# Kernel optimization log

Measured on AMD Instinct MI355X. Metric: run time of the kernel, lower is better.

## Reference

```python
import jax, jax.numpy as jnp
import numpy as np

HEAD_DIM = 64
MASK_PENALTY = 1000000.0


def setup_inputs() -> dict:
    key = jax.random.key(0)
    kq, kk, kv, ki = jax.random.split(key, 4)
    B, H, S, D = 32, 16, 512, HEAD_DIM
    E, CAP = 8, 4  # n_experts = hidden(1024)//128, capacity per expert
    Q = jax.random.normal(kq, (B, H, S, D), dtype=jnp.float32)
    K = jax.random.normal(kk, (B, H, S, D), dtype=jnp.float32)
    V = jax.random.normal(kv, (B, H, S, D), dtype=jnp.float32)
    idx_list = jax.random.randint(ki, (E, CAP), 0, B)  # per-expert routed batch indices
    mask = jnp.ones((B, S), dtype=jnp.float32)
    return {"Q": Q, "K": K, "V": V, "idx_list": idx_list, "mask": mask}


def reference(Q, K, V, idx_list, mask):
    # Per-expert grouped attention: gather routed batch rows, QK^T, masked
    # softmax, AV. Dropout is identity in eval mode.
    scale = 1.0 / jnp.sqrt(jnp.asarray(HEAD_DIM, dtype=Q.dtype))

    def expert_attn(idx_e):
        q = Q[idx_e]            # [cap, H, S, D]
        k = K[idx_e]
        v = V[idx_e]
        m = mask[idx_e]         # [cap, S]
        dot = jnp.einsum('bhsd,bhtd->bhst', q, k) * scale
        dot = dot - MASK_PENALTY * (1.0 - m[:, None, None, :])
        p = jax.nn.softmax(dot, axis=-1)
        return jnp.einsum('bhst,bhtd->bhsd', p, v)  # [cap, H, S, D]

    X = jax.vmap(expert_attn)(idx_list)  # [E, cap, H, S, D]
    return X
```

## Files before the change

kernel.cpp:

```cpp
#include <hip/hip_runtime.h>
#include <math.h>


typedef _Float16 f16x8 __attribute__((ext_vector_type(8)));
typedef _Float16 f16x4 __attribute__((ext_vector_type(4)));
typedef _Float16 f16x2 __attribute__((ext_vector_type(2)));
typedef float    f32x4 __attribute__((ext_vector_type(4)));

#define MFMA16(a, b, c) __builtin_amdgcn_mfma_f32_16x16x32_f16((a), (b), (c), 0, 0, 0)

constexpr int Hh = 16;
constexpr int Ss = 512;
constexpr int Dd = 64;
constexpr int QB = 256;
constexpr int KVB = 64;
constexpr int NT = Ss / KVB;
constexpr float QS = 0.125f * 1.44269504088896f;
constexpr float BM = 1000000.0f * 1.44269504088896f;

union U8 { f16x8 v; f16x2 h[4]; };

__device__ __forceinline__ int SW(int row, int col) {
  return row * 64 + (col ^ ((row & 7) << 3));
}

__device__ __forceinline__ f16x2 pkrtz(float a, float b) {
  auto t = __builtin_amdgcn_cvt_pkrtz(a, b);
  return *(f16x2*)&t;
}

__global__ __launch_bounds__(512) void sparse_attn_kernel(
    const float* __restrict__ Q, const float* __restrict__ K,
    const float* __restrict__ V, const int* __restrict__ idx,
    const float* __restrict__ mask, float* __restrict__ out) {
  const int tid  = threadIdx.x;
  const int lane = tid & 63;
  const int wv   = tid >> 6;
  const int r    = lane & 15;
  const int g    = lane >> 4;

  const int phys = blockIdx.x;
  const int G    = (phys & 7) | ((phys >> 4) << 3);
  const int qb   = (phys >> 3) & 1;
  const int h    = G & 15;
  const int ec   = G >> 4;
  const int b    = idx[ec];

  __shared__ _Float16 Ks[64 * 64];
  __shared__ _Float16 VTs[64 * 64];
  __shared__ float    biasS[Ss];

  const size_t bh = ((size_t)b * Hh + h) * (size_t)Ss * Dd;
  const float* Qb = Q + bh;
  const float* Kb = K + bh;
  const float* Vb = V + bh;
  const float* mrow = mask + (size_t)b * Ss;

  biasS[tid] = mrow[tid] * BM - BM;

  const int q0 = qb * QB + wv * 32;

  f16x8 qf[2][2];
#pragma unroll
  for (int mi = 0; mi < 2; ++mi)
#pragma unroll
    for (int kk = 0; kk < 2; ++kk) {
      const float* qp = Qb + (size_t)(q0 + mi * 16 + r) * Dd + kk * 32 + g * 8;
      float4 x0 = *(const float4*)qp;
      float4 x1 = *(const float4*)(qp + 4);
      U8 u;
      u.h[0] = pkrtz(x0.x * QS, x0.y * QS);
      u.h[1] = pkrtz(x0.z * QS, x0.w * QS);
      u.h[2] = pkrtz(x1.x * QS, x1.y * QS);
      u.h[3] = pkrtz(x1.z * QS, x1.w * QS);
      qf[mi][kk] = u.v;
    }

  f16x8 ones;
#pragma unroll
  for (int e = 0; e < 8; ++e) ones[e] = (_Float16)1.0f;

  f32x4 oacc[2][4];
#pragma unroll
  for (int mi = 0; mi < 2; ++mi)
#pragma unroll
    for (int nj = 0; nj < 4; ++nj) oacc[mi][nj] = (f32x4){0.f, 0.f, 0.f, 0.f};
  f32x4 lacc[2] = {(f32x4){0.f, 0.f, 0.f, 0.f}, (f32x4){0.f, 0.f, 0.f, 0.f}};

  float4 kx0, kx1;
  float  vv[8];

#define KV_ISSUE(KV0)                                                        \
  {                                                                          \
    const float* kp_ = Kb + (size_t)((KV0) + (tid >> 3)) * Dd + (tid & 7) * 8;\
    kx0 = *(const float4*)kp_;                                               \
    kx1 = *(const float4*)(kp_ + 4);                                         \
    int oct = tid >> 6;                                                      \
    int kb1 = (oct >> 2) * 16 + (oct & 3) * 4;                               \
    const float* vp = Vb + (size_t)((KV0) + kb1) * Dd + (tid & 63);          \
    _Pragma("unroll")                                                        \
    for (int jj = 0; jj < 4; ++jj) {                                         \
      vv[jj]     = vp[(size_t)jj * Dd];                                      \
      vv[jj + 4] = vp[(size_t)(jj + 32) * Dd];                               \
    }                                                                        \
  }

#define STAGE_WRITE()                                                        \
  {                                                                          \
    U8 u;                                                                    \
    u.h[0] = pkrtz(kx0.x, kx0.y);                                            \
    u.h[1] = pkrtz(kx0.z, kx0.w);                                            \
    u.h[2] = pkrtz(kx1.x, kx1.y);                                            \
    u.h[3] = pkrtz(kx1.z, kx1.w);                                            \
    *(f16x8*)&Ks[SW(tid >> 3, (tid & 7) * 8)] = u.v;                         \
    U8 u2;                                                                   \
    u2.h[0] = pkrtz(vv[0], vv[1]);                                           \
    u2.h[1] = pkrtz(vv[2], vv[3]);                                           \
    u2.h[2] = pkrtz(vv[4], vv[5]);                                           \
    u2.h[3] = pkrtz(vv[6], vv[7]);                                           \
    *(f16x8*)&VTs[SW(tid & 63, (tid >> 6) * 8)] = u2.v;                      \
  }

  KV_ISSUE(0)

  for (int t = 0; t < NT; ++t) {
    const int kv0 = t * KVB;
    if (t) __syncthreads();

    STAGE_WRITE()
    if (t < NT - 1) KV_ISSUE(kv0 + KVB)
    __syncthreads();

    f32x4 bv[4];
#pragma unroll
    for (int nj = 0; nj < 4; ++nj)
      bv[nj] = *(const f32x4*)&biasS[kv0 + nj * 16 + g * 4];

    f32x4 sf[2][4];
#pragma unroll
    for (int nj = 0; nj < 4; ++nj) { sf[0][nj] = bv[nj]; sf[1][nj] = bv[nj]; }
    __builtin_amdgcn_s_setprio(1);
#pragma unroll
    for (int nj = 0; nj < 4; ++nj)
#pragma unroll
      for (int kk = 0; kk < 2; ++kk) {
        f16x8 kf = *(const f16x8*)&Ks[SW(nj * 16 + r, kk * 32 + g * 8)];
        sf[0][nj] = MFMA16(kf, qf[0][kk], sf[0][nj]);
        sf[1][nj] = MFMA16(kf, qf[1][kk], sf[1][nj]);
      }
    __builtin_amdgcn_s_setprio(0);

    f16x8 pf[2][2];
#pragma unroll
    for (int mi = 0; mi < 2; ++mi) {
      float p[4][4];
#pragma unroll
      for (int nj = 0; nj < 4; ++nj)
#pragma unroll
        for (int rg = 0; rg < 4; ++rg)
          p[nj][rg] = __builtin_amdgcn_exp2f(sf[mi][nj][rg]);
#pragma unroll
      for (int kk = 0; kk < 2; ++kk) {
        U8 u;
        u.h[0] = pkrtz(p[kk][0], p[kk][1]);
        u.h[1] = pkrtz(p[kk][2], p[kk][3]);
        u.h[2] = pkrtz(p[kk + 2][0], p[kk + 2][1]);
        u.h[3] = pkrtz(p[kk + 2][2], p[kk + 2][3]);
        pf[mi][kk] = u.v;
      }
    }

    __builtin_amdgcn_s_setprio(1);
#pragma unroll
    for (int kk = 0; kk < 2; ++kk) {
      lacc[0] = MFMA16(pf[0][kk], ones, lacc[0]);
      lacc[1] = MFMA16(pf[1][kk], ones, lacc[1]);
#pragma unroll
      for (int nj = 0; nj < 4; ++nj) {
        f16x8 vf = *(const f16x8*)&VTs[SW(nj * 16 + r, kk * 32 + g * 8)];
        oacc[0][nj] = MFMA16(pf[0][kk], vf, oacc[0][nj]);
        oacc[1][nj] = MFMA16(pf[1][kk], vf, oacc[1][nj]);
      }
    }
    __builtin_amdgcn_s_setprio(0);
  }

  float* ob = out + ((size_t)ec * Hh + h) * (size_t)Ss * Dd;
#pragma unroll
  for (int mi = 0; mi < 2; ++mi) {
    float i4[4];
#pragma unroll
    for (int rg = 0; rg < 4; ++rg) i4[rg] = 1.0f / lacc[mi][rg];
#pragma unroll
    for (int nj = 0; nj < 4; ++nj)
#pragma unroll
      for (int rg = 0; rg < 4; ++rg) {
        int row = q0 + mi * 16 + g * 4 + rg;
        int dim = nj * 16 + r;
        ob[(size_t)row * Dd + dim] = oacc[mi][nj][rg] * i4[rg];
      }
  }
}

extern "C" void kernel_launch(void* const* d_in, const int* in_sizes, int n_in,
                              void* d_out, int out_size, void* d_ws, size_t ws_size,
                              hipStream_t stream) {
  const float* Q    = (const float*)d_in[0];
  const float* K    = (const float*)d_in[1];
  const float* V    = (const float*)d_in[2];
  const int*   idx  = (const int*)d_in[3];
  const float* mask = (const float*)d_in[4];
  float* out = (float*)d_out;
  dim3 grid(1024), block(512);
  hipLaunchKernelGGL(sparse_attn_kernel, grid, block, 0, stream,
                     Q, K, V, idx, mask, out);
}
```

Measured before the change: 65.11 us.

## Split K and V staging into separate phases to overlap with compute

Separates the K and V global-load/LDS-stage steps so V for the current tile is staged while QK^T and softmax run, and K for the next tile is staged after the PV MFMAs. K is prefetched two tiles ahead, while V gets a one-tile prefetch. The barriers are moved so each shared buffer is written only after its readers finish. This aims to hide global-load latency and barrier stalls behind MFMA work, at the cost of a more delicate sync ordering.

```diff
diff --git a/kernel.cpp b/kernel.cpp
--- a/kernel.cpp
+++ b/kernel.cpp
@@ -3,7 +3,6 @@
 
 
 typedef _Float16 f16x8 __attribute__((ext_vector_type(8)));
-typedef _Float16 f16x4 __attribute__((ext_vector_type(4)));
 typedef _Float16 f16x2 __attribute__((ext_vector_type(2)));
 typedef float    f32x4 __attribute__((ext_vector_type(4)));
 
@@ -90,11 +89,15 @@
   float4 kx0, kx1;
   float  vv[8];
 
-#define KV_ISSUE(KV0)                                                        \
+#define K_ISSUE(KV0)                                                         \
   {                                                                          \
     const float* kp_ = Kb + (size_t)((KV0) + (tid >> 3)) * Dd + (tid & 7) * 8;\
     kx0 = *(const float4*)kp_;                                               \
     kx1 = *(const float4*)(kp_ + 4);                                         \
+  }
+
+#define V_ISSUE(KV0)                                                         \
+  {                                                                          \
     int oct = tid >> 6;                                                      \
     int kb1 = (oct >> 2) * 16 + (oct & 3) * 4;                               \
     const float* vp = Vb + (size_t)((KV0) + kb1) * Dd + (tid & 63);          \
@@ -105,7 +108,7 @@
     }                                                                        \
   }
 
-#define STAGE_WRITE()                                                        \
+#define STAGE_K()                                                            \
   {                                                                          \
     U8 u;                                                                    \
     u.h[0] = pkrtz(kx0.x, kx0.y);                                            \
@@ -113,6 +116,10 @@
     u.h[2] = pkrtz(kx1.x, kx1.y);                                            \
     u.h[3] = pkrtz(kx1.z, kx1.w);                                            \
     *(f16x8*)&Ks[SW(tid >> 3, (tid & 7) * 8)] = u.v;                         \
+  }
+
+#define STAGE_V()                                                            \
+  {                                                                          \
     U8 u2;                                                                   \
     u2.h[0] = pkrtz(vv[0], vv[1]);                                           \
     u2.h[1] = pkrtz(vv[2], vv[3]);                                           \
@@ -121,24 +128,24 @@
     *(f16x8*)&VTs[SW(tid & 63, (tid >> 6) * 8)] = u2.v;                      \
   }
 
-  KV_ISSUE(0)
+  K_ISSUE(0)
+  V_ISSUE(0)
+  STAGE_K()
+  K_ISSUE(KVB)
+  __syncthreads();
 
   for (int t = 0; t < NT; ++t) {
     const int kv0 = t * KVB;
-    if (t) __syncthreads();
-
-    STAGE_WRITE()
-    if (t < NT - 1) KV_ISSUE(kv0 + KVB)
-    __syncthreads();
-
-    f32x4 bv[4];
-#pragma unroll
-    for (int nj = 0; nj < 4; ++nj)
-      bv[nj] = *(const f32x4*)&biasS[kv0 + nj * 16 + g * 4];
+
+    STAGE_V()
+    if (t < NT - 1) V_ISSUE(kv0 + KVB)
 
     f32x4 sf[2][4];
 #pragma unroll
-    for (int nj = 0; nj < 4; ++nj) { sf[0][nj] = bv[nj]; sf[1][nj] = bv[nj]; }
+    for (int nj = 0; nj < 4; ++nj) {
+      f32x4 bv = *(const f32x4*)&biasS[kv0 + nj * 16 + g * 4];
+      sf[0][nj] = bv; sf[1][nj] = bv;
+    }
     __builtin_amdgcn_s_setprio(1);
 #pragma unroll
     for (int nj = 0; nj < 4; ++nj)
@@ -169,6 +176,7 @@
         pf[mi][kk] = u.v;
       }
     }
+    __syncthreads();
 
     __builtin_amdgcn_s_setprio(1);
 #pragma unroll
@@ -183,6 +191,12 @@
       }
     }
     __builtin_amdgcn_s_setprio(0);
+
+    if (t < NT - 1) {
+      STAGE_K()
+      if (t < NT - 2) K_ISSUE(kv0 + 2 * KVB)
+      __syncthreads();
+    }
   }
 
   float* ob = out + ((size_t)ec * Hh + h) * (size_t)Ss * Dd;
```

Result: faster. 60.77 us (-6.7%).
